# Optimization experiments

Measured on AMD Instinct MI355X. Metric: run time of the kernel, lower is better.

The kernel has to match this reference:

```python
import jax, jax.numpy as jnp
import numpy as np

B, T, H, L = 64, 2048, 256, 16


def setup_inputs() -> dict:
    key = jax.random.key(0)
    ks = jax.random.split(key, 6)
    x = jax.random.normal(ks[0], (B, T, H), dtype=jnp.float32)
    tags = jax.random.randint(ks[1], (B, T), 0, L).astype(jnp.int32)
    mask = jnp.ones((B, T), dtype=bool)  # torchcrf requires mask[:,0] all on
    W = jax.random.normal(ks[2], (L, H), dtype=jnp.float32) * (1.0 / np.sqrt(H))
    b = jnp.zeros((L,), dtype=jnp.float32)
    # torchcrf initializes transitions ~ U(-0.1, 0.1)
    start_transitions = jax.random.uniform(ks[3], (L,), minval=-0.1, maxval=0.1)
    end_transitions = jax.random.uniform(ks[4], (L,), minval=-0.1, maxval=0.1)
    transitions = jax.random.uniform(ks[5], (L, L), minval=-0.1, maxval=0.1)
    return {"x": x, "W": W, "b": b,
            "start_transitions": start_transitions,
            "end_transitions": end_transitions,
            "transitions": transitions,
            "tags": tags, "mask": mask}


def reference(x, W, b, start_transitions, end_transitions, transitions, tags, mask):
    # Emitter: Linear(hidden_dim -> num_labels)
    emissions = jnp.einsum('bth,lh->btl', x, W) + b  # [B,T,L]
    maskf = mask.astype(emissions.dtype)             # [B,T]

    # ---- numerator: score of the gold tag path (vectorized, no scan) ----
    emit_gold = jnp.take_along_axis(emissions, tags[..., None].astype(jnp.int32), axis=2)[..., 0]  # [B,T]
    first_tags = tags[:, 0]
    score = start_transitions[first_tags] + emit_gold[:, 0]
    trans_gold = transitions[tags[:, :-1], tags[:, 1:]]  # [B,T-1]
    score = score + jnp.sum((trans_gold + emit_gold[:, 1:]) * maskf[:, 1:], axis=1)
    seq_ends = jnp.sum(mask.astype(jnp.int32), axis=1) - 1  # index of last valid step
    last_tags = jnp.take_along_axis(tags, seq_ends[:, None], axis=1)[:, 0]
    score = score + end_transitions[last_tags]

    # ---- denominator: forward algorithm (log partition) via lax.scan over time ----
    em_t = jnp.swapaxes(emissions, 0, 1)  # [T,B,L]
    mask_t = jnp.swapaxes(mask, 0, 1)     # [T,B]
    alpha0 = start_transitions[None, :] + em_t[0]  # [B,L]

    def step(alpha, inp):
        em, m = inp  # em: [B,L], m: [B]
        # logsumexp over previous label: alpha[b,i] + transitions[i,j] + em[b,j]
        nxt = jax.nn.logsumexp(alpha[:, :, None] + transitions[None, :, :] + em[:, None, :], axis=1)
        alpha = jnp.where(m[:, None], nxt, alpha)
        return alpha, None

    alphaT, _ = jax.lax.scan(step, alpha0, (em_t[1:], mask_t[1:]))
    denom = jax.nn.logsumexp(alphaT + end_transitions[None, :], axis=1)  # [B]

    llh = score - denom          # log-likelihood per sequence
    return -jnp.mean(llh)        # reduction='mean', nll = -crf(...)
```

## Files before the change

### kernel.cpp

```cpp
#include <hip/hip_runtime.h>
#include <math.h>


#define Bb 64
#define Tt 2048
#define Hh 256
#define Ll 16
#define CHUNK 32
#define NC (Tt / CHUNK)
#define TSTR 20

typedef __attribute__((ext_vector_type(8))) short short8;
typedef __attribute__((ext_vector_type(4))) short short4v;
typedef __attribute__((ext_vector_type(4))) float f32x4;

__device__ __forceinline__ unsigned pk2bf(float a, float b) {
  unsigned ua = __float_as_uint(a) + 0x8000u;
  unsigned ub = __float_as_uint(b) + 0x8000u;
  return (ua >> 16) | (ub & 0xFFFF0000u);
}
__device__ __forceinline__ short8 pack8(float4 lo, float4 hi) {
  union { int4 i; short8 s; } u;
  u.i.x = pk2bf(lo.x, lo.y);
  u.i.y = pk2bf(lo.z, lo.w);
  u.i.z = pk2bf(hi.x, hi.y);
  u.i.w = pk2bf(hi.z, hi.w);
  return u.s;
}

#if __has_builtin(__builtin_amdgcn_mfma_f32_16x16x16bf16_1k)
#define MFMA16(a, b, c) __builtin_amdgcn_mfma_f32_16x16x16bf16_1k(a, b, c, 0, 0, 0)
#else
__device__ __forceinline__ f32x4 mfma16_asm(short4v a, short4v b, f32x4 c) {
  f32x4 d;
  asm("v_mfma_f32_16x16x16_bf16 %0, %1, %2, %3" : "=v"(d) : "v"(a), "v"(b), "v"(c));
  return d;
}
#define MFMA16(a, b, c) mfma16_asm(a, b, c)
#endif

__device__ __forceinline__ void gload_lds16(const float* g, char* l) {
  __builtin_amdgcn_global_load_lds((const __attribute__((address_space(1))) void*)g,
                                   (__attribute__((address_space(3))) void*)l, 16, 0, 0);
}

__global__ __launch_bounds__(256, 4) void k_fused(const float* __restrict__ x,
                                                  const float* __restrict__ W,
                                                  const float* __restrict__ bias,
                                                  const float* __restrict__ strans,
                                                  const float* __restrict__ etrans,
                                                  const float* __restrict__ trans,
                                                  const int* __restrict__ tags,
                                                  float* __restrict__ em0,
                                                  float* __restrict__ Pout,
                                                  float* __restrict__ lscale,
                                                  float* __restrict__ score) {
  __shared__ __align__(16) char stage[32 * 1024];
  __shared__ float emw[CHUNK * TSTR];
  __shared__ unsigned short ghb[CHUNK * 16];
  __shared__ float Pbuf[16 * TSTR];

  const int tid = threadIdx.x, w = tid >> 6, lane = tid & 63;
  const int n = lane & 15, quad = lane >> 4;
  const int b = blockIdx.x >> 6, gc = blockIdx.x & 63;

  {
    const size_t R0 = (size_t)blockIdx.x * CHUNK;
#pragma unroll
    for (int i = 0; i < 8; ++i) {
      const int r = w * 8 + i;
      const float* src = x + (R0 + (size_t)r) * Hh + ((lane ^ (r & 7)) * 4);
      gload_lds16(src, stage + r * 1024);
    }
  }
  __syncthreads();
  if (w != 0) return;

  f32x4 acc0 = {0.f, 0.f, 0.f, 0.f}, acc1 = {0.f, 0.f, 0.f, 0.f};
  const float bs = bias[n];
  {
    const float* wbase = W + (size_t)n * Hh + quad * 8;
    short8 Bf[8];
#pragma unroll
    for (int bt = 0; bt < 2; ++bt) {
      float4 wv[8];
#pragma unroll
      for (int c2 = 0; c2 < 4; ++c2) {
        const int c = bt * 4 + c2;
        wv[2 * c2]     = *(const float4*)(wbase + c * 32);
        wv[2 * c2 + 1] = *(const float4*)(wbase + c * 32 + 4);
      }
#pragma unroll
      for (int c2 = 0; c2 < 4; ++c2) Bf[bt * 4 + c2] = pack8(wv[2 * c2], wv[2 * c2 + 1]);
    }

    const int r7 = n & 7;
    const unsigned o0 = (unsigned)((((2 * quad) ^ r7)) << 4);
    const unsigned o1 = (unsigned)((((2 * quad + 1) ^ r7)) << 4);
    const char* row0 = stage + n * 1024;
    const char* row1 = stage + (n + 16) * 1024;
#pragma unroll
    for (int c = 0; c < 8; ++c) {
      float4 v0 = *(const float4*)(row0 + 128 * c + o0);
      float4 v1 = *(const float4*)(row0 + 128 * c + o1);
      float4 u0 = *(const float4*)(row1 + 128 * c + o0);
      float4 u1 = *(const float4*)(row1 + 128 * c + o1);
      short8 a0 = pack8(v0, v1);
      short8 a1 = pack8(u0, u1);
      acc0 = __builtin_amdgcn_mfma_f32_16x16x32_bf16(a0, Bf[c], acc0, 0, 0, 0);
      acc1 = __builtin_amdgcn_mfma_f32_16x16x32_bf16(a1, Bf[c], acc1, 0, 0, 0);
    }
  }

  {
#pragma unroll
    for (int r = 0; r < 4; ++r) {
      emw[(quad * 4 + r) * TSTR + n] = acc0[r] + bs;
      emw[(16 + quad * 4 + r) * TSTR + n] = acc1[r] + bs;
    }
    if (gc == 0 && quad == 0) em0[b * 16 + n] = acc0[0] + bs;
  }

  {
    float s2 = 0.f;
    if (lane < 32) {
      int rl = lane;
      int t = gc * CHUNK + rl;
      int gt = b * Tt + t;
      int tag = tags[gt];
      float ev = emw[rl * TSTR + tag];
      if (t == 0) s2 = strans[tag] + ev;
      else        s2 = trans[tags[gt - 1] * 16 + tag] + ev;
      if (t == Tt - 1) s2 += etrans[tag];
    }
#pragma unroll
    for (int msk = 1; msk < 64; msk <<= 1) s2 += __shfl_xor(s2, msk);
    if (lane == 0) atomicAdd(score + b, s2);
  }

  float offsum = 0.f;
  {
    if (lane < 32) {
      int rl = lane;
      const float4* tp = (const float4*)(emw + rl * TSTR);
      float4 a0 = tp[0], a1 = tp[1], a2 = tp[2], a3 = tp[3];
      float m = fmaxf(fmaxf(fmaxf(fmaxf(a0.x, a0.y), fmaxf(a0.z, a0.w)),
                            fmaxf(fmaxf(a1.x, a1.y), fmaxf(a1.z, a1.w))),
                      fmaxf(fmaxf(fmaxf(a2.x, a2.y), fmaxf(a2.z, a2.w)),
                            fmaxf(fmaxf(a3.x, a3.y), fmaxf(a3.z, a3.w))));
      float4 e0 = make_float4(expf(a0.x - m), expf(a0.y - m), expf(a0.z - m), expf(a0.w - m));
      float4 e1 = make_float4(expf(a1.x - m), expf(a1.y - m), expf(a1.z - m), expf(a1.w - m));
      float4 e2 = make_float4(expf(a2.x - m), expf(a2.y - m), expf(a2.z - m), expf(a2.w - m));
      float4 e3 = make_float4(expf(a3.x - m), expf(a3.y - m), expf(a3.z - m), expf(a3.w - m));
      int4 lo, hi;
      lo.x = pk2bf(e0.x, e0.y); lo.y = pk2bf(e0.z, e0.w);
      lo.z = pk2bf(e1.x, e1.y); lo.w = pk2bf(e1.z, e1.w);
      hi.x = pk2bf(e2.x, e2.y); hi.y = pk2bf(e2.z, e2.w);
      hi.z = pk2bf(e3.x, e3.y); hi.w = pk2bf(e3.z, e3.w);
      ((int4*)ghb)[rl * 2] = lo;
      ((int4*)ghb)[rl * 2 + 1] = hi;
      int t = gc * CHUNK + rl;
      offsum = (t >= 1) ? m : 0.f;
    }
#pragma unroll
    for (int msk = 1; msk < 64; msk <<= 1) offsum += __shfl_xor(offsum, msk);
  }

  {
    union { unsigned u[2]; short4v s4; } ae;
    {
      float e0 = 0.25f * expf(trans[(quad * 4 + 0) * 16 + n]);
      float e1 = 0.25f * expf(trans[(quad * 4 + 1) * 16 + n]);
      float e2 = 0.25f * expf(trans[(quad * 4 + 2) * 16 + n]);
      float e3 = 0.25f * expf(trans[(quad * 4 + 3) * 16 + n]);
      ae.u[0] = pk2bf(e0, e1);
      ae.u[1] = pk2bf(e2, e3);
    }
    union { unsigned u[2]; short sh[4]; short4v s4; } bq;
    bq.u[0] = 0; bq.u[1] = 0;
    if ((n >> 2) == quad) bq.sh[n & 3] = (short)0x3F80;

    const int sbeg = (gc == 0) ? 1 : 0;
    const unsigned short* grow = ghb + quad * 4;
    short4v Bq = bq.s4;
    f32x4 d;
#define PSTEP(ss) { \
      const unsigned* gp = (const unsigned*)(grow + (ss) * 16); \
      unsigned glo = gp[0], ghi = gp[1]; \
      f32x4 z = {0.f, 0.f, 0.f, 0.f}; \
      d = MFMA16(ae.s4, Bq, z); \
      d[0] *= __uint_as_float(glo << 16); \
      d[1] *= __uint_as_float(glo & 0xFFFF0000u); \
      d[2] *= __uint_as_float(ghi << 16); \
      d[3] *= __uint_as_float(ghi & 0xFFFF0000u); \
      union { unsigned pu[2]; short4v ps; } pb; \
      pb.pu[0] = pk2bf(d[0], d[1]); \
      pb.pu[1] = pk2bf(d[2], d[3]); \
      Bq = pb.ps; }
    if (sbeg == 0) PSTEP(0)
#pragma unroll
    for (int s = 1; s < CHUNK; ++s) PSTEP(s)
#undef PSTEP

    float mx = fmaxf(fmaxf(d[0], d[1]), fmaxf(d[2], d[3]));
#pragma unroll
    for (int msk = 1; msk < 64; msk <<= 1) mx = fmaxf(mx, __shfl_xor(mx, msk));
    float inv = __builtin_amdgcn_rcpf(mx);
    float off = offsum + (float)(CHUNK - sbeg) * 1.3862943611198906f + logf(mx);

#pragma unroll
    for (int r = 0; r < 4; ++r) Pbuf[n * TSTR + quad * 4 + r] = d[r] * inv;
    {
      int i = lane >> 2, jg = lane & 3;
      float4 pv = *(const float4*)(Pbuf + i * TSTR + jg * 4);
      ((float4*)(Pout + ((size_t)(b * NC + gc)) * 256))[lane] = pv;
      if (lane == 0) lscale[b * NC + gc] = off;
    }
  }
}

__global__ __launch_bounds__(256) void k_combine(const float* __restrict__ em0,
                                                 const float* __restrict__ P,
                                                 const float* __restrict__ lscale,
                                                 const float* __restrict__ strans,
                                                 const float* __restrict__ etrans,
                                                 float* __restrict__ denom) {
  int b = blockIdx.x, tid = threadIdx.x;
  __shared__ float Pl[NC * 256];
  const float4* src = (const float4*)(P + (size_t)b * NC * 256);
  float4* dst = (float4*)Pl;
  for (int idx = tid; idx < NC * 64; idx += 256) dst[idx] = src[idx];
  __syncthreads();
  if (tid >= 64) return;
  int lane = tid;
  float ls = lscale[b * NC + lane];
#pragma unroll
  for (int m = 1; m < 64; m <<= 1) ls += __shfl_xor(ls, m);

  int j = lane & 15, ig = lane >> 4;
  float a = strans[j] + em0[b * 16 + j];
  float m0 = a;
#pragma unroll
  for (int m = 1; m < 16; m <<= 1) m0 = fmaxf(m0, __shfl_xor(m0, m));
  float v = expf(a - m0);
  float o = m0 + ls;

  for (int cc = 0; cc < NC; ++cc) {
    const float* Pc = Pl + cc * 256;
    float part = 0.f;
#pragma unroll
    for (int r = 0; r < 4; ++r) {
      int srcl = (ig << 4) + ig * 4 + r;
      float vr = __shfl(v, srcl);
      part = fmaf(vr, Pc[(ig * 4 + r) * 16 + j], part);
    }
    part += __shfl_xor(part, 16);
    part += __shfl_xor(part, 32);
    if ((cc & 3) == 3) {
      float mx = part;
#pragma unroll
      for (int m = 1; m < 16; m <<= 1) mx = fmaxf(mx, __shfl_xor(mx, m));
      o += logf(mx);
      v = part * __builtin_amdgcn_rcpf(mx);
    } else {
      v = part;
    }
  }
  float sj = v * expf(etrans[j]);
#pragma unroll
  for (int m = 1; m < 16; m <<= 1) sj += __shfl_xor(sj, m);
  if (lane == 0) denom[b] = o + logf(sj);
}

__global__ __launch_bounds__(64) void k_final(const float* __restrict__ score,
                                              const float* __restrict__ denom,
                                              float* __restrict__ out) {
  int lane = threadIdx.x;
  float llh = score[lane] - denom[lane];
#pragma unroll
  for (int m = 1; m < 64; m <<= 1) llh += __shfl_xor(llh, m);
  if (lane == 0) out[0] = -llh * (1.0f / 64.0f);
}

extern "C" void kernel_launch(void* const* d_in, const int* in_sizes, int n_in,
                              void* d_out, int out_size, void* d_ws, size_t ws_size,
                              hipStream_t stream) {
  const float* x = (const float*)d_in[0];
  const float* W = (const float*)d_in[1];
  const float* bias = (const float*)d_in[2];
  const float* strans = (const float*)d_in[3];
  const float* etrans = (const float*)d_in[4];
  const float* trans = (const float*)d_in[5];
  const int* tags = (const int*)d_in[6];

  float* ws = (float*)d_ws;
  float* em0 = ws;
  float* P = em0 + Bb * 16;
  float* lscale = P + (size_t)Bb * NC * 256;
  float* score = lscale + Bb * NC;
  float* denom = score + Bb;
  float* out = (float*)d_out;

  hipMemsetAsync(score, 0, Bb * sizeof(float), stream);
  hipLaunchKernelGGL(k_fused, dim3(Bb * NC), dim3(256), 0, stream,
                     x, W, bias, strans, etrans, trans, tags, em0, P, lscale, score);
  hipLaunchKernelGGL(k_combine, dim3(Bb), dim3(256), 0, stream, em0, P, lscale, strans, etrans, denom);
  hipLaunchKernelGGL(k_final, dim3(1), dim3(64), 0, stream, score, denom, out);
}
```

Measured before the change: 243.8 us.

## Use persistent single-wave blocks with double-buffered x staging across chunks

The fused kernel now launches 1024 single-wave blocks. Each block processes four consecutive 32-step chunks in 16-row halves, prefetching x into two LDS buffers via global_load_lds while it computes the emission GEMM and the chunk transfer-matrix recurrence. Previously 4096 blocks of 256 threads each had three waves that only issued loads and then exited. The W fragments, transitions and tags are loaded once per block, and the gold-path score is accumulated into a single atomic per block. The change aims to hide HBM latency behind the serial MFMA chain, at the cost of fewer resident waves and hand-managed waitcnt correctness.

```diff
diff --git a/kernel.cpp b/kernel.cpp
--- a/kernel.cpp
+++ b/kernel.cpp
@@ -44,43 +44,38 @@
                                    (__attribute__((address_space(3))) void*)l, 16, 0, 0);
 }
 
-__global__ __launch_bounds__(256, 4) void k_fused(const float* __restrict__ x,
-                                                  const float* __restrict__ W,
-                                                  const float* __restrict__ bias,
-                                                  const float* __restrict__ strans,
-                                                  const float* __restrict__ etrans,
-                                                  const float* __restrict__ trans,
-                                                  const int* __restrict__ tags,
-                                                  float* __restrict__ em0,
-                                                  float* __restrict__ Pout,
-                                                  float* __restrict__ lscale,
-                                                  float* __restrict__ score) {
-  __shared__ __align__(16) char stage[32 * 1024];
+__global__ __launch_bounds__(64) void k_fused(const float* __restrict__ x,
+                                              const float* __restrict__ W,
+                                              const float* __restrict__ bias,
+                                              const float* __restrict__ strans,
+                                              const float* __restrict__ etrans,
+                                              const float* __restrict__ trans,
+                                              const int* __restrict__ tags,
+                                              float* __restrict__ em0,
+                                              float* __restrict__ Pout,
+                                              float* __restrict__ lscale,
+                                              float* __restrict__ score) {
+  __shared__ __align__(16) char stage[2][16 * 1024];
   __shared__ float emw[CHUNK * TSTR];
-  __shared__ unsigned short ghb[CHUNK * 16];
+  __shared__ unsigned short ghb[16 * 16];
   __shared__ float Pbuf[16 * TSTR];
-
-  const int tid = threadIdx.x, w = tid >> 6, lane = tid & 63;
+  __shared__ float transL[256];
+  __shared__ float stransL[16], etransL[16];
+
+  const int lane = threadIdx.x;
   const int n = lane & 15, quad = lane >> 4;
-  const int b = blockIdx.x >> 6, gc = blockIdx.x & 63;
+  const int bid = blockIdx.x;
+  const int b = bid >> 4;
+  const size_t rowbase = (size_t)bid * 128;
 
   {
-    const size_t R0 = (size_t)blockIdx.x * CHUNK;
-#pragma unroll
-    for (int i = 0; i < 8; ++i) {
-      const int r = w * 8 + i;
-      const float* src = x + (R0 + (size_t)r) * Hh + ((lane ^ (r & 7)) * 4);
-      gload_lds16(src, stage + r * 1024);
-    }
-  }
-  __syncthreads();
-  if (w != 0) return;
-
-  f32x4 acc0 = {0.f, 0.f, 0.f, 0.f}, acc1 = {0.f, 0.f, 0.f, 0.f};
-  const float bs = bias[n];
+    float4 tv = ((const float4*)trans)[lane];
+    ((float4*)transL)[lane] = tv;
+    if (lane < 16) { stransL[lane] = strans[lane]; etransL[lane] = etrans[lane]; }
+  }
+  short8 Bf[8];
   {
     const float* wbase = W + (size_t)n * Hh + quad * 8;
-    short8 Bf[8];
 #pragma unroll
     for (int bt = 0; bt < 2; ++bt) {
       float4 wv[8];
@@ -93,130 +88,163 @@
 #pragma unroll
       for (int c2 = 0; c2 < 4; ++c2) Bf[bt * 4 + c2] = pack8(wv[2 * c2], wv[2 * c2 + 1]);
     }
-
-    const int r7 = n & 7;
-    const unsigned o0 = (unsigned)((((2 * quad) ^ r7)) << 4);
-    const unsigned o1 = (unsigned)((((2 * quad + 1) ^ r7)) << 4);
-    const char* row0 = stage + n * 1024;
-    const char* row1 = stage + (n + 16) * 1024;
-#pragma unroll
-    for (int c = 0; c < 8; ++c) {
-      float4 v0 = *(const float4*)(row0 + 128 * c + o0);
-      float4 v1 = *(const float4*)(row0 + 128 * c + o1);
-      float4 u0 = *(const float4*)(row1 + 128 * c + o0);
-      float4 u1 = *(const float4*)(row1 + 128 * c + o1);
-      short8 a0 = pack8(v0, v1);
-      short8 a1 = pack8(u0, u1);
-      acc0 = __builtin_amdgcn_mfma_f32_16x16x32_bf16(a0, Bf[c], acc0, 0, 0, 0);
-      acc1 = __builtin_amdgcn_mfma_f32_16x16x32_bf16(a1, Bf[c], acc1, 0, 0, 0);
-    }
-  }
-
+  }
+  const float bs = bias[n];
+  asm volatile("s_waitcnt lgkmcnt(0)" ::: "memory");
+  union { unsigned u[2]; short4v s4; } ae;
   {
-#pragma unroll
-    for (int r = 0; r < 4; ++r) {
-      emw[(quad * 4 + r) * TSTR + n] = acc0[r] + bs;
-      emw[(16 + quad * 4 + r) * TSTR + n] = acc1[r] + bs;
-    }
-    if (gc == 0 && quad == 0) em0[b * 16 + n] = acc0[0] + bs;
-  }
-
-  {
-    float s2 = 0.f;
-    if (lane < 32) {
-      int rl = lane;
-      int t = gc * CHUNK + rl;
-      int gt = b * Tt + t;
-      int tag = tags[gt];
-      float ev = emw[rl * TSTR + tag];
-      if (t == 0) s2 = strans[tag] + ev;
-      else        s2 = trans[tags[gt - 1] * 16 + tag] + ev;
-      if (t == Tt - 1) s2 += etrans[tag];
-    }
-#pragma unroll
-    for (int msk = 1; msk < 64; msk <<= 1) s2 += __shfl_xor(s2, msk);
-    if (lane == 0) atomicAdd(score + b, s2);
-  }
-
-  float offsum = 0.f;
-  {
-    if (lane < 32) {
-      int rl = lane;
-      const float4* tp = (const float4*)(emw + rl * TSTR);
-      float4 a0 = tp[0], a1 = tp[1], a2 = tp[2], a3 = tp[3];
-      float m = fmaxf(fmaxf(fmaxf(fmaxf(a0.x, a0.y), fmaxf(a0.z, a0.w)),
-                            fmaxf(fmaxf(a1.x, a1.y), fmaxf(a1.z, a1.w))),
-                      fmaxf(fmaxf(fmaxf(a2.x, a2.y), fmaxf(a2.z, a2.w)),
-                            fmaxf(fmaxf(a3.x, a3.y), fmaxf(a3.z, a3.w))));
-      float4 e0 = make_float4(expf(a0.x - m), expf(a0.y - m), expf(a0.z - m), expf(a0.w - m));
-      float4 e1 = make_float4(expf(a1.x - m), expf(a1.y - m), expf(a1.z - m), expf(a1.w - m));
-      float4 e2 = make_float4(expf(a2.x - m), expf(a2.y - m), expf(a2.z - m), expf(a2.w - m));
-      float4 e3 = make_float4(expf(a3.x - m), expf(a3.y - m), expf(a3.z - m), expf(a3.w - m));
-      int4 lo, hi;
-      lo.x = pk2bf(e0.x, e0.y); lo.y = pk2bf(e0.z, e0.w);
-      lo.z = pk2bf(e1.x, e1.y); lo.w = pk2bf(e1.z, e1.w);
-      hi.x = pk2bf(e2.x, e2.y); hi.y = pk2bf(e2.z, e2.w);
-      hi.z = pk2bf(e3.x, e3.y); hi.w = pk2bf(e3.z, e3.w);
-      ((int4*)ghb)[rl * 2] = lo;
-      ((int4*)ghb)[rl * 2 + 1] = hi;
-      int t = gc * CHUNK + rl;
-      offsum = (t >= 1) ? m : 0.f;
-    }
-#pragma unroll
-    for (int msk = 1; msk < 64; msk <<= 1) offsum += __shfl_xor(offsum, msk);
-  }
-
-  {
-    union { unsigned u[2]; short4v s4; } ae;
-    {
-      float e0 = 0.25f * expf(trans[(quad * 4 + 0) * 16 + n]);
-      float e1 = 0.25f * expf(trans[(quad * 4 + 1) * 16 + n]);
-      float e2 = 0.25f * expf(trans[(quad * 4 + 2) * 16 + n]);
-      float e3 = 0.25f * expf(trans[(quad * 4 + 3) * 16 + n]);
-      ae.u[0] = pk2bf(e0, e1);
-      ae.u[1] = pk2bf(e2, e3);
-    }
+    float e0 = 0.25f * expf(transL[(quad * 4 + 0) * 16 + n]);
+    float e1 = 0.25f * expf(transL[(quad * 4 + 1) * 16 + n]);
+    float e2 = 0.25f * expf(transL[(quad * 4 + 2) * 16 + n]);
+    float e3 = 0.25f * expf(transL[(quad * 4 + 3) * 16 + n]);
+    ae.u[0] = pk2bf(e0, e1);
+    ae.u[1] = pk2bf(e2, e3);
+  }
+
+#define STAGE(H) { \
+    const size_t gr_ = rowbase + (size_t)(H) * 16; \
+    char* lb_ = stage[(H) & 1]; \
+    _Pragma("unroll") \
+    for (int r_ = 0; r_ < 16; ++r_) { \
+      const float* sp_ = x + (gr_ + r_) * Hh + ((lane ^ (r_ & 7)) * 4); \
+      gload_lds16(sp_, lb_ + r_ * 1024); \
+    } }
+
+  STAGE(0)
+  STAGE(1)
+
+  const int r7 = n & 7;
+  const unsigned o0 = (unsigned)(((2 * quad) ^ r7) << 4);
+  const unsigned o1 = (unsigned)(((2 * quad + 1) ^ r7) << 4);
+  float s2 = 0.f;
+
+  for (int it = 0; it < 4; ++it) {
+    const int C = bid * 4 + it;
+    const int cb = C * CHUNK;
     union { unsigned u[2]; short sh[4]; short4v s4; } bq;
     bq.u[0] = 0; bq.u[1] = 0;
     if ((n >> 2) == quad) bq.sh[n & 3] = (short)0x3F80;
-
-    const int sbeg = (gc == 0) ? 1 : 0;
-    const unsigned short* grow = ghb + quad * 4;
     short4v Bq = bq.s4;
     f32x4 d;
+    float offsum = 0.f;
+    int tagc = 0, tagp = 0;
+
+#pragma unroll
+    for (int h = 0; h < 2; ++h) {
+      if (it == 3 && h == 1) { asm volatile("s_waitcnt vmcnt(0)" ::: "memory"); }
+      else                   { asm volatile("s_waitcnt vmcnt(16)" ::: "memory"); }
+      __builtin_amdgcn_sched_barrier(0);
+
+      if (h == 0) {
+        int li = cb + lane;
+        if (lane < 32) {
+          tagc = tags[li];
+          tagp = tags[(li > 0) ? (li - 1) : 0];
+        }
+      }
+
+      const char* bufh = stage[h];
+      f32x4 acc = {0.f, 0.f, 0.f, 0.f};
+#pragma unroll
+      for (int c = 0; c < 8; ++c) {
+        float4 v0 = *(const float4*)(bufh + n * 1024 + c * 128 + o0);
+        float4 v1 = *(const float4*)(bufh + n * 1024 + c * 128 + o1);
+        acc = __builtin_amdgcn_mfma_f32_16x16x32_bf16(pack8(v0, v1), Bf[c], acc, 0, 0, 0);
+      }
+      asm volatile("s_waitcnt lgkmcnt(0)" ::: "memory");
+      __builtin_amdgcn_sched_barrier(0);
+      if (it < 3) STAGE(it * 2 + h + 2)
+
+#pragma unroll
+      for (int r = 0; r < 4; ++r)
+        emw[(h * 16 + quad * 4 + r) * TSTR + n] = acc[r] + bs;
+      if ((bid & 15) == 0 && it == 0 && h == 0 && quad == 0)
+        em0[(bid >> 4) * 16 + n] = acc[0] + bs;
+
+      {
+        float mh = 0.f;
+        if (lane < 16) {
+          const float4* tp = (const float4*)(emw + (h * 16 + lane) * TSTR);
+          float4 a0 = tp[0], a1 = tp[1], a2 = tp[2], a3 = tp[3];
+          float m = fmaxf(fmaxf(fmaxf(fmaxf(a0.x, a0.y), fmaxf(a0.z, a0.w)),
+                                fmaxf(fmaxf(a1.x, a1.y), fmaxf(a1.z, a1.w))),
+                          fmaxf(fmaxf(fmaxf(a2.x, a2.y), fmaxf(a2.z, a2.w)),
+                                fmaxf(fmaxf(a3.x, a3.y), fmaxf(a3.z, a3.w))));
+          float4 e0 = make_float4(expf(a0.x - m), expf(a0.y - m), expf(a0.z - m), expf(a0.w - m));
+          float4 e1 = make_float4(expf(a1.x - m), expf(a1.y - m), expf(a1.z - m), expf(a1.w - m));
+          float4 e2 = make_float4(expf(a2.x - m), expf(a2.y - m), expf(a2.z - m), expf(a2.w - m));
+          float4 e3 = make_float4(expf(a3.x - m), expf(a3.y - m), expf(a3.z - m), expf(a3.w - m));
+          int4 lo, hi;
+          lo.x = pk2bf(e0.x, e0.y); lo.y = pk2bf(e0.z, e0.w);
+          lo.z = pk2bf(e1.x, e1.y); lo.w = pk2bf(e1.z, e1.w);
+          hi.x = pk2bf(e2.x, e2.y); hi.y = pk2bf(e2.z, e2.w);
+          hi.z = pk2bf(e3.x, e3.y); hi.w = pk2bf(e3.z, e3.w);
+          ((int4*)ghb)[lane * 2] = lo;
+          ((int4*)ghb)[lane * 2 + 1] = hi;
+          int t = cb + h * 16 + lane;
+          mh = (t >= 1) ? m : 0.f;
+        }
+#pragma unroll
+        for (int msk = 1; msk < 64; msk <<= 1) mh += __shfl_xor(mh, msk);
+        offsum += mh;
+      }
+
+      {
+        const unsigned short* grow = ghb + quad * 4;
 #define PSTEP(ss) { \
-      const unsigned* gp = (const unsigned*)(grow + (ss) * 16); \
-      unsigned glo = gp[0], ghi = gp[1]; \
-      f32x4 z = {0.f, 0.f, 0.f, 0.f}; \
-      d = MFMA16(ae.s4, Bq, z); \
-      d[0] *= __uint_as_float(glo << 16); \
-      d[1] *= __uint_as_float(glo & 0xFFFF0000u); \
-      d[2] *= __uint_as_float(ghi << 16); \
-      d[3] *= __uint_as_float(ghi & 0xFFFF0000u); \
-      union { unsigned pu[2]; short4v ps; } pb; \
-      pb.pu[0] = pk2bf(d[0], d[1]); \
-      pb.pu[1] = pk2bf(d[2], d[3]); \
-      Bq = pb.ps; }
-    if (sbeg == 0) PSTEP(0)
-#pragma unroll
-    for (int s = 1; s < CHUNK; ++s) PSTEP(s)
+        const unsigned* gp = (const unsigned*)(grow + (ss) * 16); \
+        unsigned glo = gp[0], ghi = gp[1]; \
+        f32x4 z = {0.f, 0.f, 0.f, 0.f}; \
+        d = MFMA16(ae.s4, Bq, z); \
+        d[0] *= __uint_as_float(glo << 16); \
+        d[1] *= __uint_as_float(glo & 0xFFFF0000u); \
+        d[2] *= __uint_as_float(ghi << 16); \
+        d[3] *= __uint_as_float(ghi & 0xFFFF0000u); \
+        union { unsigned pu[2]; short4v ps; } pb; \
+        pb.pu[0] = pk2bf(d[0], d[1]); \
+        pb.pu[1] = pk2bf(d[2], d[3]); \
+        Bq = pb.ps; }
+        if (h == 0) {
+          if (C != 0) PSTEP(0)
+#pragma unroll
+          for (int s = 1; s < 16; ++s) PSTEP(s)
+        } else {
+#pragma unroll
+          for (int s = 0; s < 16; ++s) PSTEP(s)
+        }
 #undef PSTEP
-
-    float mx = fmaxf(fmaxf(d[0], d[1]), fmaxf(d[2], d[3]));
-#pragma unroll
-    for (int msk = 1; msk < 64; msk <<= 1) mx = fmaxf(mx, __shfl_xor(mx, msk));
-    float inv = __builtin_amdgcn_rcpf(mx);
-    float off = offsum + (float)(CHUNK - sbeg) * 1.3862943611198906f + logf(mx);
-
-#pragma unroll
-    for (int r = 0; r < 4; ++r) Pbuf[n * TSTR + quad * 4 + r] = d[r] * inv;
+      }
+    }
+
+    if (lane < 32) {
+      int t = cb + lane;
+      float ev = emw[lane * TSTR + tagc];
+      float c2 = (t == 0) ? (stransL[tagc] + ev) : (transL[tagp * 16 + tagc] + ev);
+      if (t == Tt - 1) c2 += etransL[tagc];
+      s2 += c2;
+    }
+
     {
+      float mx = fmaxf(fmaxf(d[0], d[1]), fmaxf(d[2], d[3]));
+#pragma unroll
+      for (int msk = 1; msk < 64; msk <<= 1) mx = fmaxf(mx, __shfl_xor(mx, msk));
+      float inv = __builtin_amdgcn_rcpf(mx);
+      int nsteps = (C == 0) ? (CHUNK - 1) : CHUNK;
+      float off = offsum + (float)nsteps * 1.3862943611198906f + logf(mx);
+
+#pragma unroll
+      for (int r = 0; r < 4; ++r) Pbuf[n * TSTR + quad * 4 + r] = d[r] * inv;
       int i = lane >> 2, jg = lane & 3;
       float4 pv = *(const float4*)(Pbuf + i * TSTR + jg * 4);
-      ((float4*)(Pout + ((size_t)(b * NC + gc)) * 256))[lane] = pv;
-      if (lane == 0) lscale[b * NC + gc] = off;
-    }
-  }
+      ((float4*)(Pout + ((size_t)C) * 256))[lane] = pv;
+      if (lane == 0) lscale[C] = off;
+    }
+  }
+
+#pragma unroll
+  for (int msk = 1; msk < 64; msk <<= 1) s2 += __shfl_xor(s2, msk);
+  if (lane == 0) atomicAdd(score + b, s2);
+#undef STAGE
 }
 
 __global__ __launch_bounds__(256) void k_combine(const float* __restrict__ em0,
@@ -302,7 +330,7 @@
   float* out = (float*)d_out;
 
   hipMemsetAsync(score, 0, Bb * sizeof(float), stream);
-  hipLaunchKernelGGL(k_fused, dim3(Bb * NC), dim3(256), 0, stream,
+  hipLaunchKernelGGL(k_fused, dim3(1024), dim3(64), 0, stream,
                      x, W, bias, strans, etrans, trans, tags, em0, P, lscale, score);
   hipLaunchKernelGGL(k_combine, dim3(Bb), dim3(256), 0, stream, em0, P, lscale, strans, etrans, denom);
   hipLaunchKernelGGL(k_final, dim3(1), dim3(64), 0, stream, score, denom, out);
```

New measurement: 234.9 us. -3.7%, faster.

## Give every wave its own 64-row slab with register double-buffered x loads

Applied to the files above, without the earlier changes.

Previously each block loaded a 32-row chunk into LDS and then only wave 0 did the work while three waves exited. Now all four waves each own 64 rows (two 32-step chunks), with W staged once per block in LDS. Each wave streams x through registers in 16-row groups, prefetching the next group while it runs the MFMA GEMM and the 16-step transfer-matrix scan on the current one. The grid shrinks from 4096 to 512 blocks and launch bounds drop to 2 blocks per CU, which trades occupancy and more register pressure for better wave utilisation and overlap of load with compute.

```diff
diff --git a/kernel.cpp b/kernel.cpp
--- a/kernel.cpp
+++ b/kernel.cpp
@@ -39,12 +39,7 @@
 #define MFMA16(a, b, c) mfma16_asm(a, b, c)
 #endif
 
-__device__ __forceinline__ void gload_lds16(const float* g, char* l) {
-  __builtin_amdgcn_global_load_lds((const __attribute__((address_space(1))) void*)g,
-                                   (__attribute__((address_space(3))) void*)l, 16, 0, 0);
-}
-
-__global__ __launch_bounds__(256, 4) void k_fused(const float* __restrict__ x,
+__global__ __launch_bounds__(256, 2) void k_fused(const float* __restrict__ x,
                                                   const float* __restrict__ W,
                                                   const float* __restrict__ bias,
                                                   const float* __restrict__ strans,
@@ -55,168 +50,187 @@
                                                   float* __restrict__ Pout,
                                                   float* __restrict__ lscale,
                                                   float* __restrict__ score) {
-  __shared__ __align__(16) char stage[32 * 1024];
-  __shared__ float emw[CHUNK * TSTR];
-  __shared__ unsigned short ghb[CHUNK * 16];
-  __shared__ float Pbuf[16 * TSTR];
+  __shared__ __align__(16) char stageS[4][16 * 1024];
+  __shared__ float emwS[4][16 * TSTR];
+  __shared__ unsigned short ghbS[4][16 * 16];
+  __shared__ __align__(16) char WL[8192];
 
   const int tid = threadIdx.x, w = tid >> 6, lane = tid & 63;
   const int n = lane & 15, quad = lane >> 4;
-  const int b = blockIdx.x >> 6, gc = blockIdx.x & 63;
-
+  const int wg = blockIdx.x * 4 + w;
+  const size_t rowbase = (size_t)wg * 64;
+  const int b = (int)(rowbase >> 11);
+
+  if (w == 0) {
+    const float* wbase = W + (size_t)n * Hh + quad * 8;
+    float4 wv[16];
+#pragma unroll
+    for (int c = 0; c < 8; ++c) {
+      wv[2 * c] = *(const float4*)(wbase + c * 32);
+      wv[2 * c + 1] = *(const float4*)(wbase + c * 32 + 4);
+    }
+#pragma unroll
+    for (int c = 0; c < 8; ++c) {
+      short8 f = pack8(wv[2 * c], wv[2 * c + 1]);
+      *(short8*)(WL + (c * 4 + quad) * 256 + n * 16) = f;
+    }
+  }
+  const float bs = bias[n];
+  union { unsigned u[2]; short4v s4; } ae;
   {
-    const size_t R0 = (size_t)blockIdx.x * CHUNK;
-#pragma unroll
-    for (int i = 0; i < 8; ++i) {
-      const int r = w * 8 + i;
-      const float* src = x + (R0 + (size_t)r) * Hh + ((lane ^ (r & 7)) * 4);
-      gload_lds16(src, stage + r * 1024);
-    }
+    float e0 = 0.25f * expf(trans[(quad * 4 + 0) * 16 + n]);
+    float e1 = 0.25f * expf(trans[(quad * 4 + 1) * 16 + n]);
+    float e2 = 0.25f * expf(trans[(quad * 4 + 2) * 16 + n]);
+    float e3 = 0.25f * expf(trans[(quad * 4 + 3) * 16 + n]);
+    ae.u[0] = pk2bf(e0, e1);
+    ae.u[1] = pk2bf(e2, e3);
+  }
+  int tc0 = 0, tp0 = 0, tc1 = 0, tp1 = 0;
+  if (lane < 32) {
+    size_t g0 = rowbase + lane, g1 = rowbase + 32 + lane;
+    tc0 = tags[g0]; tp0 = tags[(g0 > 0) ? (g0 - 1) : 0];
+    tc1 = tags[g1]; tp1 = tags[g1 - 1];
   }
   __syncthreads();
-  if (w != 0) return;
-
-  f32x4 acc0 = {0.f, 0.f, 0.f, 0.f}, acc1 = {0.f, 0.f, 0.f, 0.f};
-  const float bs = bias[n];
-  {
-    const float* wbase = W + (size_t)n * Hh + quad * 8;
-    short8 Bf[8];
-#pragma unroll
-    for (int bt = 0; bt < 2; ++bt) {
-      float4 wv[8];
-#pragma unroll
-      for (int c2 = 0; c2 < 4; ++c2) {
-        const int c = bt * 4 + c2;
-        wv[2 * c2]     = *(const float4*)(wbase + c * 32);
-        wv[2 * c2 + 1] = *(const float4*)(wbase + c * 32 + 4);
-      }
-#pragma unroll
-      for (int c2 = 0; c2 < 4; ++c2) Bf[bt * 4 + c2] = pack8(wv[2 * c2], wv[2 * c2 + 1]);
-    }
-
-    const int r7 = n & 7;
-    const unsigned o0 = (unsigned)((((2 * quad) ^ r7)) << 4);
-    const unsigned o1 = (unsigned)((((2 * quad + 1) ^ r7)) << 4);
-    const char* row0 = stage + n * 1024;
-    const char* row1 = stage + (n + 16) * 1024;
-#pragma unroll
-    for (int c = 0; c < 8; ++c) {
-      float4 v0 = *(const float4*)(row0 + 128 * c + o0);
-      float4 v1 = *(const float4*)(row0 + 128 * c + o1);
-      float4 u0 = *(const float4*)(row1 + 128 * c + o0);
-      float4 u1 = *(const float4*)(row1 + 128 * c + o1);
-      short8 a0 = pack8(v0, v1);
-      short8 a1 = pack8(u0, u1);
-      acc0 = __builtin_amdgcn_mfma_f32_16x16x32_bf16(a0, Bf[c], acc0, 0, 0, 0);
-      acc1 = __builtin_amdgcn_mfma_f32_16x16x32_bf16(a1, Bf[c], acc1, 0, 0, 0);
-    }
-  }
-
-  {
-#pragma unroll
-    for (int r = 0; r < 4; ++r) {
-      emw[(quad * 4 + r) * TSTR + n] = acc0[r] + bs;
-      emw[(16 + quad * 4 + r) * TSTR + n] = acc1[r] + bs;
-    }
-    if (gc == 0 && quad == 0) em0[b * 16 + n] = acc0[0] + bs;
-  }
-
-  {
-    float s2 = 0.f;
-    if (lane < 32) {
-      int rl = lane;
-      int t = gc * CHUNK + rl;
-      int gt = b * Tt + t;
-      int tag = tags[gt];
-      float ev = emw[rl * TSTR + tag];
-      if (t == 0) s2 = strans[tag] + ev;
-      else        s2 = trans[tags[gt - 1] * 16 + tag] + ev;
-      if (t == Tt - 1) s2 += etrans[tag];
-    }
-#pragma unroll
-    for (int msk = 1; msk < 64; msk <<= 1) s2 += __shfl_xor(s2, msk);
-    if (lane == 0) atomicAdd(score + b, s2);
-  }
-
-  float offsum = 0.f;
-  {
-    if (lane < 32) {
-      int rl = lane;
-      const float4* tp = (const float4*)(emw + rl * TSTR);
-      float4 a0 = tp[0], a1 = tp[1], a2 = tp[2], a3 = tp[3];
-      float m = fmaxf(fmaxf(fmaxf(fmaxf(a0.x, a0.y), fmaxf(a0.z, a0.w)),
-                            fmaxf(fmaxf(a1.x, a1.y), fmaxf(a1.z, a1.w))),
-                      fmaxf(fmaxf(fmaxf(a2.x, a2.y), fmaxf(a2.z, a2.w)),
-                            fmaxf(fmaxf(a3.x, a3.y), fmaxf(a3.z, a3.w))));
-      float4 e0 = make_float4(expf(a0.x - m), expf(a0.y - m), expf(a0.z - m), expf(a0.w - m));
-      float4 e1 = make_float4(expf(a1.x - m), expf(a1.y - m), expf(a1.z - m), expf(a1.w - m));
-      float4 e2 = make_float4(expf(a2.x - m), expf(a2.y - m), expf(a2.z - m), expf(a2.w - m));
-      float4 e3 = make_float4(expf(a3.x - m), expf(a3.y - m), expf(a3.z - m), expf(a3.w - m));
-      int4 lo, hi;
-      lo.x = pk2bf(e0.x, e0.y); lo.y = pk2bf(e0.z, e0.w);
-      lo.z = pk2bf(e1.x, e1.y); lo.w = pk2bf(e1.z, e1.w);
-      hi.x = pk2bf(e2.x, e2.y); hi.y = pk2bf(e2.z, e2.w);
-      hi.z = pk2bf(e3.x, e3.y); hi.w = pk2bf(e3.z, e3.w);
-      ((int4*)ghb)[rl * 2] = lo;
-      ((int4*)ghb)[rl * 2 + 1] = hi;
-      int t = gc * CHUNK + rl;
-      offsum = (t >= 1) ? m : 0.f;
-    }
-#pragma unroll
-    for (int msk = 1; msk < 64; msk <<= 1) offsum += __shfl_xor(offsum, msk);
-  }
-
-  {
-    union { unsigned u[2]; short4v s4; } ae;
-    {
-      float e0 = 0.25f * expf(trans[(quad * 4 + 0) * 16 + n]);
-      float e1 = 0.25f * expf(trans[(quad * 4 + 1) * 16 + n]);
-      float e2 = 0.25f * expf(trans[(quad * 4 + 2) * 16 + n]);
-      float e3 = 0.25f * expf(trans[(quad * 4 + 3) * 16 + n]);
-      ae.u[0] = pk2bf(e0, e1);
-      ae.u[1] = pk2bf(e2, e3);
-    }
+
+  char* stg = stageS[w];
+  float* emw = emwS[w];
+  unsigned short* ghb = ghbS[w];
+
+#define LOADB(bi, ra) _Pragma("unroll") \
+    for (int k_ = 0; k_ < 8; ++k_) \
+      ra[k_] = *(const float4*)(x + (rowbase + (size_t)((bi) * 8 + k_)) * Hh + lane * 4);
+#define WRITEB(bi, ra) _Pragma("unroll") \
+    for (int k_ = 0; k_ < 8; ++k_) { \
+      int rm_ = (((bi) & 1) * 8) + k_; \
+      *(float4*)(stg + rm_ * 1024 + ((lane ^ (rm_ & 7)) << 4)) = ra[k_]; \
+    }
+
+  float4 raA[8], raB[8];
+  LOADB(0, raA)
+  LOADB(1, raB)
+
+  const int r7 = n & 7;
+  const unsigned o0 = (unsigned)(((2 * quad) ^ r7) << 4);
+  const unsigned o1 = (unsigned)(((2 * quad + 1) ^ r7) << 4);
+  const int tb0 = (int)(rowbase & 2047);
+  float s2 = 0.f;
+
+  for (int ic = 0; ic < 2; ++ic) {
+    const int tbase = tb0 + ic * 32;
+    const int Cg = wg * 2 + ic;
     union { unsigned u[2]; short sh[4]; short4v s4; } bq;
     bq.u[0] = 0; bq.u[1] = 0;
     if ((n >> 2) == quad) bq.sh[n & 3] = (short)0x3F80;
-
-    const int sbeg = (gc == 0) ? 1 : 0;
-    const unsigned short* grow = ghb + quad * 4;
     short4v Bq = bq.s4;
     f32x4 d;
+    float offsum = 0.f;
+
+#pragma unroll
+    for (int hm = 0; hm < 2; ++hm) {
+      const int mg = ic * 2 + hm;
+      WRITEB(2 * mg, raA)
+      WRITEB(2 * mg + 1, raB)
+      if (mg < 3) {
+        LOADB(2 * mg + 2, raA)
+        LOADB(2 * mg + 3, raB)
+      }
+
+      f32x4 acc = {0.f, 0.f, 0.f, 0.f};
+#pragma unroll
+      for (int c = 0; c < 8; ++c) {
+        float4 v0 = *(const float4*)(stg + n * 1024 + c * 128 + o0);
+        float4 v1 = *(const float4*)(stg + n * 1024 + c * 128 + o1);
+        short8 bf = *(const short8*)(WL + (c * 4 + quad) * 256 + n * 16);
+        acc = __builtin_amdgcn_mfma_f32_16x16x32_bf16(pack8(v0, v1), bf, acc, 0, 0, 0);
+      }
+#pragma unroll
+      for (int r = 0; r < 4; ++r) emw[(quad * 4 + r) * TSTR + n] = acc[r] + bs;
+      if (tbase == 0 && hm == 0 && quad == 0) em0[b * 16 + n] = acc[0] + bs;
+
+      {
+        float mh = 0.f;
+        if (lane < 16) {
+          const float4* tp4 = (const float4*)(emw + lane * TSTR);
+          float4 a0 = tp4[0], a1 = tp4[1], a2 = tp4[2], a3 = tp4[3];
+          float m = fmaxf(fmaxf(fmaxf(fmaxf(a0.x, a0.y), fmaxf(a0.z, a0.w)),
+                                fmaxf(fmaxf(a1.x, a1.y), fmaxf(a1.z, a1.w))),
+                          fmaxf(fmaxf(fmaxf(a2.x, a2.y), fmaxf(a2.z, a2.w)),
+                                fmaxf(fmaxf(a3.x, a3.y), fmaxf(a3.z, a3.w))));
+          float4 e0 = make_float4(expf(a0.x - m), expf(a0.y - m), expf(a0.z - m), expf(a0.w - m));
+          float4 e1 = make_float4(expf(a1.x - m), expf(a1.y - m), expf(a1.z - m), expf(a1.w - m));
+          float4 e2 = make_float4(expf(a2.x - m), expf(a2.y - m), expf(a2.z - m), expf(a2.w - m));
+          float4 e3 = make_float4(expf(a3.x - m), expf(a3.y - m), expf(a3.z - m), expf(a3.w - m));
+          int4 lo, hi;
+          lo.x = pk2bf(e0.x, e0.y); lo.y = pk2bf(e0.z, e0.w);
+          lo.z = pk2bf(e1.x, e1.y); lo.w = pk2bf(e1.z, e1.w);
+          hi.x = pk2bf(e2.x, e2.y); hi.y = pk2bf(e2.z, e2.w);
+          hi.z = pk2bf(e3.x, e3.y); hi.w = pk2bf(e3.z, e3.w);
+          ((int4*)ghb)[lane * 2] = lo;
+          ((int4*)ghb)[lane * 2 + 1] = hi;
+          int t = tbase + hm * 16 + lane;
+          mh = (t >= 1) ? m : 0.f;
+        }
+#pragma unroll
+        for (int msk = 1; msk < 64; msk <<= 1) mh += __shfl_xor(mh, msk);
+        offsum += mh;
+      }
+
+      if (lane < 32 && (lane >> 4) == hm) {
+        int tagc = ic ? tc1 : tc0;
+        int tagp = ic ? tp1 : tp0;
+        int t = tbase + lane;
+        float ev = emw[(lane & 15) * TSTR + tagc];
+        float c2 = (t == 0) ? (strans[tagc] + ev) : (trans[tagp * 16 + tagc] + ev);
+        if (t == Tt - 1) c2 += etrans[tagc];
+        s2 += c2;
+      }
+
+      {
+        const unsigned short* grow = ghb + quad * 4;
 #define PSTEP(ss) { \
-      const unsigned* gp = (const unsigned*)(grow + (ss) * 16); \
-      unsigned glo = gp[0], ghi = gp[1]; \
-      f32x4 z = {0.f, 0.f, 0.f, 0.f}; \
-      d = MFMA16(ae.s4, Bq, z); \
-      d[0] *= __uint_as_float(glo << 16); \
-      d[1] *= __uint_as_float(glo & 0xFFFF0000u); \
-      d[2] *= __uint_as_float(ghi << 16); \
-      d[3] *= __uint_as_float(ghi & 0xFFFF0000u); \
-      union { unsigned pu[2]; short4v ps; } pb; \
-      pb.pu[0] = pk2bf(d[0], d[1]); \
-      pb.pu[1] = pk2bf(d[2], d[3]); \
-      Bq = pb.ps; }
-    if (sbeg == 0) PSTEP(0)
-#pragma unroll
-    for (int s = 1; s < CHUNK; ++s) PSTEP(s)
+        const unsigned* gp = (const unsigned*)(grow + (ss) * 16); \
+        unsigned glo = gp[0], ghi = gp[1]; \
+        f32x4 z = {0.f, 0.f, 0.f, 0.f}; \
+        d = MFMA16(ae.s4, Bq, z); \
+        d[0] *= __uint_as_float(glo << 16); \
+        d[1] *= __uint_as_float(glo & 0xFFFF0000u); \
+        d[2] *= __uint_as_float(ghi << 16); \
+        d[3] *= __uint_as_float(ghi & 0xFFFF0000u); \
+        union { unsigned pu[2]; short4v ps; } pb; \
+        pb.pu[0] = pk2bf(d[0], d[1]); \
+        pb.pu[1] = pk2bf(d[2], d[3]); \
+        Bq = pb.ps; }
+        if (!(tbase == 0 && hm == 0)) PSTEP(0)
+#pragma unroll
+        for (int s = 1; s < 16; ++s) PSTEP(s)
 #undef PSTEP
-
-    float mx = fmaxf(fmaxf(d[0], d[1]), fmaxf(d[2], d[3]));
-#pragma unroll
-    for (int msk = 1; msk < 64; msk <<= 1) mx = fmaxf(mx, __shfl_xor(mx, msk));
-    float inv = __builtin_amdgcn_rcpf(mx);
-    float off = offsum + (float)(CHUNK - sbeg) * 1.3862943611198906f + logf(mx);
-
-#pragma unroll
-    for (int r = 0; r < 4; ++r) Pbuf[n * TSTR + quad * 4 + r] = d[r] * inv;
+      }
+    }
+
     {
+      float mx = fmaxf(fmaxf(d[0], d[1]), fmaxf(d[2], d[3]));
+#pragma unroll
+      for (int msk = 1; msk < 64; msk <<= 1) mx = fmaxf(mx, __shfl_xor(mx, msk));
+      float inv = __builtin_amdgcn_rcpf(mx);
+      int nsteps = (tbase == 0) ? (CHUNK - 1) : CHUNK;
+      float off = offsum + (float)nsteps * 1.3862943611198906f + logf(mx);
+
+      float* Pb = emw;
+#pragma unroll
+      for (int r = 0; r < 4; ++r) Pb[n * TSTR + quad * 4 + r] = d[r] * inv;
       int i = lane >> 2, jg = lane & 3;
-      float4 pv = *(const float4*)(Pbuf + i * TSTR + jg * 4);
-      ((float4*)(Pout + ((size_t)(b * NC + gc)) * 256))[lane] = pv;
-      if (lane == 0) lscale[b * NC + gc] = off;
-    }
-  }
+      float4 pv = *(const float4*)(Pb + i * TSTR + jg * 4);
+      ((float4*)(Pout + (size_t)Cg * 256))[lane] = pv;
+      if (lane == 0) lscale[Cg] = off;
+    }
+  }
+
+#pragma unroll
+  for (int msk = 1; msk < 64; msk <<= 1) s2 += __shfl_xor(s2, msk);
+  if (lane == 0) atomicAdd(score + b, s2);
+#undef LOADB
+#undef WRITEB
 }
 
 __global__ __launch_bounds__(256) void k_combine(const float* __restrict__ em0,
@@ -302,7 +316,7 @@
   float* out = (float*)d_out;
 
   hipMemsetAsync(score, 0, Bb * sizeof(float), stream);
-  hipLaunchKernelGGL(k_fused, dim3(Bb * NC), dim3(256), 0, stream,
+  hipLaunchKernelGGL(k_fused, dim3(512), dim3(256), 0, stream,
                      x, W, bias, strans, etrans, trans, tags, em0, P, lscale, score);
   hipLaunchKernelGGL(k_combine, dim3(Bb), dim3(256), 0, stream, em0, P, lscale, strans, etrans, denom);
   hipLaunchKernelGGL(k_final, dim3(1), dim3(64), 0, stream, score, denom, out);
```

New measurement: 248.5 us. About the same (+1.9%).
